# Kernel tuning notes

Hardware: AMD Instinct MI355X
Metric: run time of the kernel (lower is better)

The kernel has to match this reference:

```python
import jax, jax.numpy as jnp
import numpy as np

K = 5       # local window size (== scale, so patches are non-overlapping)
SCALE = 5


def setup_inputs() -> dict:
    key = jax.random.key(0)
    k1, k2, k3, k4, k5 = jax.random.split(key, 5)
    B, C, H, W = 4, 64, 128, 128
    feat_q = jax.random.normal(k1, (B, C, H, W), dtype=jnp.float32)
    feat_kv = jax.random.normal(k2, (B, C, H * SCALE, W * SCALE), dtype=jnp.float32)
    s = 0.05
    Wq = jax.random.normal(k3, (C, C), dtype=jnp.float32) * s
    Wk = jax.random.normal(k4, (C, C), dtype=jnp.float32) * s
    Wv = jax.random.normal(k5, (C, C), dtype=jnp.float32) * s
    return {"feat_q": feat_q, "feat_kv": feat_kv, "Wq": Wq, "Wk": Wk, "Wv": Wv}


def _patches(x, B, C, H, W):
    # nn.Unfold(kernel=K, stride=SCALE) with K == SCALE -> non-overlapping KxK
    # blocks, flattened channel-major as (C, kh, kw): [B, C, K*K, H*W]
    x = x.reshape(B, C, H, K, W, K)
    x = x.transpose(0, 1, 3, 5, 2, 4)  # [B, C, K, K, H, W]
    return x.reshape(B, C, K * K, H * W)


def reference(feat_q, feat_kv, Wq, Wk, Wv):
    B, C, H, W = feat_q.shape
    # 1x1 conv projections == channel matmuls
    q = jnp.einsum('oc,bchw->bohw', Wq, feat_q)
    k = jnp.einsum('oc,bchw->bohw', Wk, feat_kv)
    v = jnp.einsum('oc,bchw->bohw', Wv, feat_kv)
    kp = _patches(k, B, C, H, W)   # [B, C, K*K, HW]
    vp = _patches(v, B, C, H, W)   # [B, C, K*K, HW]
    qf = q.reshape(B, C, H * W)    # [B, C, HW]
    # attn[b, l, n] = sum_c q[b,c,l] * k[b,c,n,l]
    attn = jnp.einsum('bcl,bcnl->bln', qf, kp) / jnp.sqrt(jnp.float32(C))
    attn = jax.nn.softmax(attn, axis=-1)
    out = jnp.einsum('bln,bcnl->bcl', attn, vp).reshape(B, C, H, W)
    return feat_q + out
```

## Files before the change

### kernel.cpp

```cpp
#include <hip/hip_runtime.h>

namespace {

constexpr int C = 64, H = 128, W = 128, K5 = 5, HK = 640, WK = 640;
constexpr int PIX = 16;
constexpr int XD = 80;
constexpr int THREADS = 512;
constexpr int XPAD = 84;
constexpr int CP = 68;
constexpr int LP = 33;

__device__ inline unsigned int packbf2(float lo, float hi) {
    unsigned int a = __float_as_uint(lo), b = __float_as_uint(hi);
    a = (a + 0x7FFFu + ((a >> 16) & 1u)) >> 16;
    b = (b + 0x7FFFu + ((b >> 16) & 1u)) & 0xFFFF0000u;
    return a | b;
}
__device__ inline float blo(unsigned int u) { return __uint_as_float(u << 16); }
__device__ inline float bhi(unsigned int u) { return __uint_as_float(u & 0xFFFF0000u); }

__global__ void prep_wqk(const float* __restrict__ Wq, const float* __restrict__ Wk,
                         float* __restrict__ Wqk) {
    int tid = blockIdx.x * 256 + threadIdx.x;
    int i = tid >> 6, j = tid & 63;
    float acc = 0.f;
    #pragma unroll 8
    for (int c = 0; c < 64; ++c) acc = fmaf(Wk[c * 64 + i], Wq[c * 64 + j], acc);
    Wqk[i * 64 + j] = 0.125f * acc;
}

__global__ __launch_bounds__(THREADS, 4)
void cag_main(const float* __restrict__ fq, const float* __restrict__ fkv,
              const float* __restrict__ Wv, const float* __restrict__ Wqk,
              float* __restrict__ out) {
    __shared__ unsigned int slab[K5 * 32 * XPAD];
    __shared__ float fq_lds[PIX * CP];
    __shared__ float qk_lds[PIX * CP];
    __shared__ float lg[PIX * LP];
    __shared__ float wsum[PIX * CP];

    const int t = threadIdx.x;
    const int bid = blockIdx.x;
    const int wb = bid & 7;
    const int h  = (bid >> 3) & 127;
    const int b  = bid >> 10;
    const int row0 = K5 * h, col0 = XD * wb, w0q = PIX * wb;

    {
        const float* kvb = fkv + (size_t)b * C * HK * WK;
        const size_t CSTR = (size_t)HK * WK;
        for (int i = t; i < 1600; i += THREADS) {
            int x4 = i % 20;
            int y  = (i / 20) % 5;
            int c4 = i / 100;
            const float* g = kvb + ((size_t)(4 * c4) * HK + (row0 + y)) * WK + col0 + 4 * x4;
            float4 F0 = *(const float4*)(g);
            float4 F1 = *(const float4*)(g + CSTR);
            float4 F2 = *(const float4*)(g + 2 * CSTR);
            float4 F3 = *(const float4*)(g + 3 * CSTR);
            unsigned int* r0 = &slab[(y * 32 + 2 * c4) * XPAD + 4 * x4];
            unsigned int* r1 = r0 + XPAD;
            *(uint4*)r0 = make_uint4(packbf2(F0.x, F1.x), packbf2(F0.y, F1.y),
                                     packbf2(F0.z, F1.z), packbf2(F0.w, F1.w));
            *(uint4*)r1 = make_uint4(packbf2(F2.x, F3.x), packbf2(F2.y, F3.y),
                                     packbf2(F2.z, F3.z), packbf2(F2.w, F3.w));
        }
    }
    {
        int p = t & 15, c = t >> 4;
        fq_lds[p * CP + c]      = fq[((size_t)(b * C + c) * H + h) * W + w0q + p];
        fq_lds[p * CP + c + 32] = fq[((size_t)(b * C + c + 32) * H + h) * W + w0q + p];
    }
    __syncthreads();

    {
        int l = t & 15, i0 = t >> 4;
        const float4* wr0 = (const float4*)(Wqk + i0 * 64);
        const float4* wr1 = (const float4*)(Wqk + (i0 + 32) * 64);
        const float4* fv  = (const float4*)(fq_lds + l * CP);
        float a0 = 0.f, a1 = 0.f;
        #pragma unroll
        for (int j = 0; j < 16; ++j) {
            float4 f = fv[j], w0 = wr0[j], w1 = wr1[j];
            a0 = fmaf(w0.x, f.x, a0); a0 = fmaf(w0.y, f.y, a0);
            a0 = fmaf(w0.z, f.z, a0); a0 = fmaf(w0.w, f.w, a0);
            a1 = fmaf(w1.x, f.x, a1); a1 = fmaf(w1.y, f.y, a1);
            a1 = fmaf(w1.z, f.z, a1); a1 = fmaf(w1.w, f.w, a1);
        }
        qk_lds[l * CP + i0]      = a0;
        qk_lds[l * CP + i0 + 32] = a1;
    }
    __syncthreads();

    {
        int n = t & 31, l = t >> 5;
        if (n < 25) {
            int ky = n / 5, kx = n - 5 * ky;
            int x = 5 * l + kx;
            const unsigned int* sp = &slab[(ky * 32) * XPAD + x];
            const float4* qv = (const float4*)(qk_lds + l * CP);
            float acc = 0.f;
            #pragma unroll
            for (int q4 = 0; q4 < 8; ++q4) {
                float4 qa = qv[2 * q4], qb = qv[2 * q4 + 1];
                unsigned int s0 = sp[(4 * q4 + 0) * XPAD];
                unsigned int s1 = sp[(4 * q4 + 1) * XPAD];
                unsigned int s2 = sp[(4 * q4 + 2) * XPAD];
                unsigned int s3 = sp[(4 * q4 + 3) * XPAD];
                acc = fmaf(qa.x, blo(s0), acc); acc = fmaf(qa.y, bhi(s0), acc);
                acc = fmaf(qa.z, blo(s1), acc); acc = fmaf(qa.w, bhi(s1), acc);
                acc = fmaf(qb.x, blo(s2), acc); acc = fmaf(qb.y, bhi(s2), acc);
                acc = fmaf(qb.z, blo(s3), acc); acc = fmaf(qb.w, bhi(s3), acc);
            }
            lg[l * LP + n] = acc;
        }
    }
    __syncthreads();

    {
        int lane = t & 63, w = t >> 6;
        int n = lane & 31;
        int l = 2 * w + (lane >> 5);
        float v = (n < 25) ? lg[l * LP + n] : -1e30f;
        float m = v;
        #pragma unroll
        for (int off = 16; off; off >>= 1) m = fmaxf(m, __shfl_xor(m, off, 32));
        float e = __expf(v - m);
        float s = e;
        #pragma unroll
        for (int off = 16; off; off >>= 1) s += __shfl_xor(s, off, 32);
        if (n < 25) lg[l * LP + n] = e / s;
    }
    __syncthreads();

    {
        int l = t & 15, icp = t >> 4;
        float alo = 0.f, ahi = 0.f;
        #pragma unroll
        for (int n = 0; n < 25; ++n) {
            const int ky = n / 5, kx = n - 5 * ky;
            float a = lg[l * LP + n];
            unsigned int s = slab[(ky * 32 + icp) * XPAD + 5 * l + kx];
            alo = fmaf(a, blo(s), alo);
            ahi = fmaf(a, bhi(s), ahi);
        }
        wsum[l * CP + 2 * icp]     = alo;
        wsum[l * CP + 2 * icp + 1] = ahi;
    }
    __syncthreads();

    {
        int p = t & 15, o0 = t >> 4;
        const float4* wv0 = (const float4*)(Wv + o0 * 64);
        const float4* wv1 = (const float4*)(Wv + (o0 + 32) * 64);
        const float4* ws  = (const float4*)(wsum + p * CP);
        float a0 = 0.f, a1 = 0.f;
        #pragma unroll
        for (int j = 0; j < 16; ++j) {
            float4 f = ws[j], w0 = wv0[j], w1 = wv1[j];
            a0 = fmaf(w0.x, f.x, a0); a0 = fmaf(w0.y, f.y, a0);
            a0 = fmaf(w0.z, f.z, a0); a0 = fmaf(w0.w, f.w, a0);
            a1 = fmaf(w1.x, f.x, a1); a1 = fmaf(w1.y, f.y, a1);
            a1 = fmaf(w1.z, f.z, a1); a1 = fmaf(w1.w, f.w, a1);
        }
        size_t ob = ((size_t)(b * C + o0) * H + h) * W + w0q + p;
        out[ob]                    = fq_lds[p * CP + o0]      + a0;
        out[ob + (size_t)32 * H * W] = fq_lds[p * CP + o0 + 32] + a1;
    }
}

}

extern "C" void kernel_launch(void* const* d_in, const int* in_sizes, int n_in,
                              void* d_out, int out_size, void* d_ws, size_t ws_size,
                              hipStream_t stream) {
    (void)in_sizes; (void)n_in; (void)ws_size; (void)out_size;
    const float* fq  = (const float*)d_in[0];
    const float* fkv = (const float*)d_in[1];
    const float* Wq  = (const float*)d_in[2];
    const float* Wk  = (const float*)d_in[3];
    const float* Wv  = (const float*)d_in[4];
    float* out = (float*)d_out;
    float* Wqk = (float*)d_ws;

    prep_wqk<<<dim3(16), dim3(256), 0, stream>>>(Wq, Wk, Wqk);
    cag_main<<<dim3(4 * 128 * 8), dim3(THREADS), 0, stream>>>(fq, fkv, Wv, Wqk, out);
}
```

Before: 147.0 us.

## Split fused attention kernel into projection, attention, and output-projection kernels

Breaks the single fused kernel into three: a per-pixel q·Wqk projection written as bf16 to workspace, an attention kernel that loads the KV slab into a swizzled channel-contiguous LDS layout and writes bf16 weighted sums, and a per-pixel Wv output projection with residual add. The intent is to lower LDS use and register pressure in the heavy attention kernel so occupancy rises, and to make its LDS reads vectorized and bank-conflict-free. The cost is extra global round trips through workspace, two more launches, and additional bf16 rounding of q and of the weighted sums.

```diff
diff --git a/kernel.cpp b/kernel.cpp
--- a/kernel.cpp
+++ b/kernel.cpp
@@ -2,13 +2,9 @@
 
 namespace {
 
-constexpr int C = 64, H = 128, W = 128, K5 = 5, HK = 640, WK = 640;
-constexpr int PIX = 16;
-constexpr int XD = 80;
+constexpr int C = 64, H = 128, W = 128, HK = 640, WK = 640;
+constexpr long long CSTR = (long long)HK * WK;
 constexpr int THREADS = 512;
-constexpr int XPAD = 84;
-constexpr int CP = 68;
-constexpr int LP = 33;
 
 __device__ inline unsigned int packbf2(float lo, float hi) {
     unsigned int a = __float_as_uint(lo), b = __float_as_uint(hi);
@@ -29,99 +25,97 @@
     Wqk[i * 64 + j] = 0.125f * acc;
 }
 
-__global__ __launch_bounds__(THREADS, 4)
-void cag_main(const float* __restrict__ fq, const float* __restrict__ fkv,
-              const float* __restrict__ Wv, const float* __restrict__ Wqk,
-              float* __restrict__ out) {
-    __shared__ unsigned int slab[K5 * 32 * XPAD];
-    __shared__ float fq_lds[PIX * CP];
-    __shared__ float qk_lds[PIX * CP];
-    __shared__ float lg[PIX * LP];
-    __shared__ float wsum[PIX * CP];
+__global__ __launch_bounds__(256)
+void qk_proj(const float* __restrict__ fq, const float* __restrict__ Wqk,
+             unsigned int* __restrict__ qk_g) {
+    const int pix = blockIdx.x * 256 + threadIdx.x;
+    const int b = pix >> 14, l = pix & 16383;
+    float col[64];
+    #pragma unroll
+    for (int c = 0; c < 64; ++c)
+        col[c] = fq[((size_t)(b * 64 + c) << 14) + l];
+    #pragma unroll 2
+    for (int i4 = 0; i4 < 16; ++i4) {
+        float a0 = 0.f, a1 = 0.f, a2 = 0.f, a3 = 0.f;
+        #pragma unroll
+        for (int j = 0; j < 64; ++j) {
+            float f = col[j];
+            a0 = fmaf(Wqk[(4 * i4 + 0) * 64 + j], f, a0);
+            a1 = fmaf(Wqk[(4 * i4 + 1) * 64 + j], f, a1);
+            a2 = fmaf(Wqk[(4 * i4 + 2) * 64 + j], f, a2);
+            a3 = fmaf(Wqk[(4 * i4 + 3) * 64 + j], f, a3);
+        }
+        uint2 u = make_uint2(packbf2(a0, a1), packbf2(a2, a3));
+        *(uint2*)&qk_g[(size_t)pix * 32 + 2 * i4] = u;
+    }
+}
+
+__global__ __launch_bounds__(THREADS, 6)
+void cag_attn(const float* __restrict__ fkv, const unsigned int* __restrict__ qk_g,
+              unsigned int* __restrict__ wsum_g) {
+    __shared__ unsigned int slab[5 * 80 * 32];
+    __shared__ float lg[16 * 26];
 
     const int t = threadIdx.x;
     const int bid = blockIdx.x;
     const int wb = bid & 7;
     const int h  = (bid >> 3) & 127;
     const int b  = bid >> 10;
-    const int row0 = K5 * h, col0 = XD * wb, w0q = PIX * wb;
+    const int row0 = 5 * h, col0 = 80 * wb;
+    const int pix0 = h * 128 + 16 * wb;
 
     {
-        const float* kvb = fkv + (size_t)b * C * HK * WK;
-        const size_t CSTR = (size_t)HK * WK;
+        const float* kvb = fkv + (size_t)b * C * CSTR;
         for (int i = t; i < 1600; i += THREADS) {
-            int x4 = i % 20;
-            int y  = (i / 20) % 5;
-            int c4 = i / 100;
-            const float* g = kvb + ((size_t)(4 * c4) * HK + (row0 + y)) * WK + col0 + 4 * x4;
+            const int x4s = i & 3;
+            const int c4  = (i >> 2) & 15;
+            const int rem = i >> 6;
+            const int y   = rem % 5;
+            const int x4g = rem / 5;
+            const int xb  = 16 * x4g + 4 * x4s;
+            const float* g = kvb + (size_t)(4 * c4) * CSTR
+                           + (size_t)(row0 + y) * WK + (col0 + xb);
             float4 F0 = *(const float4*)(g);
             float4 F1 = *(const float4*)(g + CSTR);
             float4 F2 = *(const float4*)(g + 2 * CSTR);
             float4 F3 = *(const float4*)(g + 3 * CSTR);
-            unsigned int* r0 = &slab[(y * 32 + 2 * c4) * XPAD + 4 * x4];
-            unsigned int* r1 = r0 + XPAD;
-            *(uint4*)r0 = make_uint4(packbf2(F0.x, F1.x), packbf2(F0.y, F1.y),
-                                     packbf2(F0.z, F1.z), packbf2(F0.w, F1.w));
-            *(uint4*)r1 = make_uint4(packbf2(F2.x, F3.x), packbf2(F2.y, F3.y),
-                                     packbf2(F2.z, F3.z), packbf2(F2.w, F3.w));
-        }
-    }
-    {
-        int p = t & 15, c = t >> 4;
-        fq_lds[p * CP + c]      = fq[((size_t)(b * C + c) * H + h) * W + w0q + p];
-        fq_lds[p * CP + c + 32] = fq[((size_t)(b * C + c + 32) * H + h) * W + w0q + p];
-    }
-    __syncthreads();
-
-    {
-        int l = t & 15, i0 = t >> 4;
-        const float4* wr0 = (const float4*)(Wqk + i0 * 64);
-        const float4* wr1 = (const float4*)(Wqk + (i0 + 32) * 64);
-        const float4* fv  = (const float4*)(fq_lds + l * CP);
-        float a0 = 0.f, a1 = 0.f;
-        #pragma unroll
-        for (int j = 0; j < 16; ++j) {
-            float4 f = fv[j], w0 = wr0[j], w1 = wr1[j];
-            a0 = fmaf(w0.x, f.x, a0); a0 = fmaf(w0.y, f.y, a0);
-            a0 = fmaf(w0.z, f.z, a0); a0 = fmaf(w0.w, f.w, a0);
-            a1 = fmaf(w1.x, f.x, a1); a1 = fmaf(w1.y, f.y, a1);
-            a1 = fmaf(w1.z, f.z, a1); a1 = fmaf(w1.w, f.w, a1);
-        }
-        qk_lds[l * CP + i0]      = a0;
-        qk_lds[l * CP + i0 + 32] = a1;
-    }
-    __syncthreads();
-
-    {
-        int n = t & 31, l = t >> 5;
-        if (n < 25) {
-            int ky = n / 5, kx = n - 5 * ky;
-            int x = 5 * l + kx;
-            const unsigned int* sp = &slab[(ky * 32) * XPAD + x];
-            const float4* qv = (const float4*)(qk_lds + l * CP);
-            float acc = 0.f;
+            const float* f0 = (const float*)&F0; const float* f1 = (const float*)&F1;
+            const float* f2 = (const float*)&F2; const float* f3 = (const float*)&F3;
             #pragma unroll
-            for (int q4 = 0; q4 < 8; ++q4) {
-                float4 qa = qv[2 * q4], qb = qv[2 * q4 + 1];
-                unsigned int s0 = sp[(4 * q4 + 0) * XPAD];
-                unsigned int s1 = sp[(4 * q4 + 1) * XPAD];
-                unsigned int s2 = sp[(4 * q4 + 2) * XPAD];
-                unsigned int s3 = sp[(4 * q4 + 3) * XPAD];
-                acc = fmaf(qa.x, blo(s0), acc); acc = fmaf(qa.y, bhi(s0), acc);
-                acc = fmaf(qa.z, blo(s1), acc); acc = fmaf(qa.w, bhi(s1), acc);
-                acc = fmaf(qb.x, blo(s2), acc); acc = fmaf(qb.y, bhi(s2), acc);
-                acc = fmaf(qb.z, blo(s3), acc); acc = fmaf(qb.w, bhi(s3), acc);
+            for (int dx = 0; dx < 4; ++dx) {
+                const int x = xb + dx;
+                const int base = (y * 80 + x) * 32;
+                const int sw = (((x & 7) ^ y) << 2);
+                slab[base + ((2 * c4)     ^ sw)] = packbf2(f0[dx], f1[dx]);
+                slab[base + ((2 * c4 + 1) ^ sw)] = packbf2(f2[dx], f3[dx]);
             }
-            lg[l * LP + n] = acc;
         }
     }
     __syncthreads();
 
+    const int l = t >> 5;
+    const int n = t & 31;
+
     {
-        int lane = t & 63, w = t >> 6;
-        int n = lane & 31;
-        int l = 2 * w + (lane >> 5);
-        float v = (n < 25) ? lg[l * LP + n] : -1e30f;
+        float v = -1e30f;
+        if (n < 25) {
+            const int ky = n / 5, kx = n - 5 * (n / 5);
+            const int x = 5 * l + kx;
+            const int base = (ky * 80 + x) * 32;
+            const int sw7 = (x & 7) ^ ky;
+            const uint4* qkr = (const uint4*)(qk_g + ((size_t)b * 16384 + pix0 + l) * 32);
+            float acc = 0.f;
+            #pragma unroll
+            for (int j = 0; j < 8; ++j) {
+                uint4 u = *(const uint4*)&slab[base + 4 * (j ^ sw7)];
+                uint4 q = qkr[j];
+                acc = fmaf(blo(q.x), blo(u.x), acc); acc = fmaf(bhi(q.x), bhi(u.x), acc);
+                acc = fmaf(blo(q.y), blo(u.y), acc); acc = fmaf(bhi(q.y), bhi(u.y), acc);
+                acc = fmaf(blo(q.z), blo(u.z), acc); acc = fmaf(bhi(q.z), bhi(u.z), acc);
+                acc = fmaf(blo(q.w), blo(u.w), acc); acc = fmaf(bhi(q.w), bhi(u.w), acc);
+            }
+            v = acc;
+        }
         float m = v;
         #pragma unroll
         for (int off = 16; off; off >>= 1) m = fmaxf(m, __shfl_xor(m, off, 32));
@@ -129,43 +123,51 @@
         float s = e;
         #pragma unroll
         for (int off = 16; off; off >>= 1) s += __shfl_xor(s, off, 32);
-        if (n < 25) lg[l * LP + n] = e / s;
+        if (n < 25) lg[l * 26 + n] = e / s;
     }
     __syncthreads();
 
     {
-        int l = t & 15, icp = t >> 4;
+        const int s = t & 31;
         float alo = 0.f, ahi = 0.f;
         #pragma unroll
-        for (int n = 0; n < 25; ++n) {
-            const int ky = n / 5, kx = n - 5 * ky;
-            float a = lg[l * LP + n];
-            unsigned int s = slab[(ky * 32 + icp) * XPAD + 5 * l + kx];
-            alo = fmaf(a, blo(s), alo);
-            ahi = fmaf(a, bhi(s), ahi);
+        for (int n2 = 0; n2 < 25; ++n2) {
+            const int ky = n2 / 5, kx = n2 - 5 * ky;
+            const int x = 5 * l + kx;
+            const unsigned int u = slab[(ky * 80 + x) * 32 + (s ^ ((((x & 7) ^ ky)) << 2))];
+            const float a = lg[l * 26 + n2];
+            alo = fmaf(a, blo(u), alo);
+            ahi = fmaf(a, bhi(u), ahi);
         }
-        wsum[l * CP + 2 * icp]     = alo;
-        wsum[l * CP + 2 * icp + 1] = ahi;
+        wsum_g[((size_t)b * 16384 + pix0 + l) * 32 + s] = packbf2(alo, ahi);
     }
-    __syncthreads();
+}
 
-    {
-        int p = t & 15, o0 = t >> 4;
-        const float4* wv0 = (const float4*)(Wv + o0 * 64);
-        const float4* wv1 = (const float4*)(Wv + (o0 + 32) * 64);
-        const float4* ws  = (const float4*)(wsum + p * CP);
-        float a0 = 0.f, a1 = 0.f;
+__global__ __launch_bounds__(256)
+void out_proj(const float* __restrict__ fq, const float* __restrict__ Wv,
+              const unsigned int* __restrict__ wsum_g, float* __restrict__ out) {
+    const int pix = blockIdx.x * 256 + threadIdx.x;
+    const int b = pix >> 14, l = pix & 16383;
+    float vals[64];
+    #pragma unroll
+    for (int g8 = 0; g8 < 8; ++g8) {
+        uint4 u = *(const uint4*)&wsum_g[(size_t)pix * 32 + 4 * g8];
+        const unsigned int us[4] = {u.x, u.y, u.z, u.w};
         #pragma unroll
-        for (int j = 0; j < 16; ++j) {
-            float4 f = ws[j], w0 = wv0[j], w1 = wv1[j];
-            a0 = fmaf(w0.x, f.x, a0); a0 = fmaf(w0.y, f.y, a0);
-            a0 = fmaf(w0.z, f.z, a0); a0 = fmaf(w0.w, f.w, a0);
-            a1 = fmaf(w1.x, f.x, a1); a1 = fmaf(w1.y, f.y, a1);
-            a1 = fmaf(w1.z, f.z, a1); a1 = fmaf(w1.w, f.w, a1);
+        for (int c2 = 0; c2 < 4; ++c2) {
+            const int s = 4 * g8 + c2;
+            const int ic0 = 4 * (s >> 1) + 2 * (s & 1);
+            vals[ic0]     = blo(us[c2]);
+            vals[ic0 + 1] = bhi(us[c2]);
         }
-        size_t ob = ((size_t)(b * C + o0) * H + h) * W + w0q + p;
-        out[ob]                    = fq_lds[p * CP + o0]      + a0;
-        out[ob + (size_t)32 * H * W] = fq_lds[p * CP + o0 + 32] + a1;
+    }
+    #pragma unroll 2
+    for (int oc = 0; oc < 64; ++oc) {
+        float acc = fq[((size_t)(b * 64 + oc) << 14) + l];
+        #pragma unroll
+        for (int ic = 0; ic < 64; ++ic)
+            acc = fmaf(Wv[oc * 64 + ic], vals[ic], acc);
+        out[((size_t)(b * 64 + oc) << 14) + l] = acc;
     }
 }
 
@@ -181,8 +183,13 @@
     const float* Wk  = (const float*)d_in[3];
     const float* Wv  = (const float*)d_in[4];
     float* out = (float*)d_out;
+
     float* Wqk = (float*)d_ws;
+    unsigned int* qk_g   = (unsigned int*)((char*)d_ws + 16384);
+    unsigned int* wsum_g = (unsigned int*)((char*)d_ws + 16384 + 8388608);
 
-    prep_wqk<<<dim3(16), dim3(256), 0, stream>>>(Wq, Wk, Wqk);
-    cag_main<<<dim3(4 * 128 * 8), dim3(THREADS), 0, stream>>>(fq, fkv, Wv, Wqk, out);
+    prep_wqk<<<dim3(16),   dim3(256), 0, stream>>>(Wq, Wk, Wqk);
+    qk_proj <<<dim3(256),  dim3(256), 0, stream>>>(fq, Wqk, qk_g);
+    cag_attn<<<dim3(4096), dim3(THREADS), 0, stream>>>(fkv, qk_g, wsum_g);
+    out_proj<<<dim3(256),  dim3(256), 0, stream>>>(fq, Wv, wsum_g, out);
 }
```

Measured after the change: 232.8 us. 58.4% more time.
